# Kernel optimization log

Hardware: AMD Instinct MI355X
Metric: run time of the kernel (lower is better)

The kernel has to match this reference:

```python
import jax, jax.numpy as jnp
import numpy as np

B, C, H, W = 2, 192, 128, 128
NUM_HEADS = 6
AMP = 1
NUM_OFFSETS = 9


def bilinear_sample(img, grid):
    # img: (C, H, W); grid: (Hn, Wn, 2) in [-1,1], align_corners=True, zeros padding
    Hh, Ww = img.shape[1], img.shape[2]
    x = (grid[..., 0] + 1.0) * 0.5 * (Ww - 1)
    y = (grid[..., 1] + 1.0) * 0.5 * (Hh - 1)
    x0 = jnp.floor(x)
    y0 = jnp.floor(y)
    x1 = x0 + 1.0
    y1 = y0 + 1.0
    wx1 = x - x0
    wy1 = y - y0

    def gather(yi, xi):
        valid = ((xi >= 0) & (xi <= Ww - 1) & (yi >= 0) & (yi <= Hh - 1)).astype(img.dtype)
        xc = jnp.clip(xi, 0, Ww - 1).astype(jnp.int32)
        yc = jnp.clip(yi, 0, Hh - 1).astype(jnp.int32)
        return img[:, yc, xc] * valid  # (C, Hn, Wn)

    return (gather(y0, x0) * ((1 - wy1) * (1 - wx1))
            + gather(y0, x1) * ((1 - wy1) * wx1)
            + gather(y1, x0) * (wy1 * (1 - wx1))
            + gather(y1, x1) * (wy1 * wx1))


def setup_inputs() -> dict:
    key = jax.random.key(0)
    ks = jax.random.split(key, 8)
    s = 0.02
    Ch = C // NUM_HEADS
    return {
        "x_q": jax.random.normal(ks[0], (B, C, H, W), jnp.float32),
        "x_kv": jax.random.normal(ks[1], (B, C, H, W), jnp.float32),
        "w_q": jax.random.normal(ks[2], (C, C), jnp.float32) * s,
        "w_kv": jax.random.normal(ks[3], (2 * C, C), jnp.float32) * s,
        "w_off1": jax.random.normal(ks[4], (C, 2 * C, 3, 3), jnp.float32) * s,
        "b_off1": jnp.zeros((C,), jnp.float32),
        "w_off2": jax.random.normal(ks[5], (2 * NUM_OFFSETS, C), jnp.float32) * s,
        "b_off2": jnp.zeros((2 * NUM_OFFSETS,), jnp.float32),
        "w_proj": jax.random.normal(ks[6], (C, C), jnp.float32) * s,
        "b_proj": jnp.zeros((C,), jnp.float32),
    }


def reference(x_q, x_kv, w_q, w_kv, w_off1, b_off1, w_off2, b_off2, w_proj, b_proj):
    Ch = C // NUM_HEADS
    scale = Ch ** (-0.5)

    # 1x1 conv projections as channel matmuls
    q = jnp.einsum('oc,bchw->bohw', w_q, x_q) * scale
    kv = jnp.einsum('oc,bchw->bohw', w_kv, x_kv)
    k, v = kv[:, :C], kv[:, C:]  # kv.reshape(B,2,Ch,nh,H,W) -> first C channels are k

    # offset predictor: 3x3 conv -> relu -> 1x1 conv
    off_in = jnp.concatenate([x_q, x_kv], axis=1)
    h1 = jax.lax.conv_general_dilated(off_in, w_off1, (1, 1), 'SAME',
                                      dimension_numbers=('NCHW', 'OIHW', 'NCHW'))
    h1 = jax.nn.relu(h1 + b_off1[None, :, None, None])
    off = jnp.einsum('oc,bchw->bohw', w_off2, h1) + b_off2[None, :, None, None]
    off = off.reshape(B, NUM_OFFSETS, 2, H, W).transpose(0, 1, 3, 4, 2)  # (B,9,H,W,2)
    gx = off[..., 0] / (W - 1) * 2.0 - 1.0
    gy = off[..., 1] / (H - 1) * 2.0 - 1.0
    grid = jnp.stack([gx, gy], axis=-1)  # (B,9,H,W,2)

    # deformable gather: sample full-channel k/v at each of 9 per-pixel offset grids
    sample = jax.vmap(jax.vmap(bilinear_sample, in_axes=(None, 0)), in_axes=(0, 0))
    k_s = sample(k, grid).reshape(B, NUM_OFFSETS, Ch, NUM_HEADS, H, W)
    v_s = sample(v, grid).reshape(B, NUM_OFFSETS, Ch, NUM_HEADS, H, W)

    q = q.reshape(B, Ch, NUM_HEADS, H, W)

    pad = [(0, 0), (0, 0), (0, 0), (0, 0), (AMP, AMP), (AMP, AMP)]
    k_p = jnp.pad(k_s, pad)
    v_p = jnp.pad(v_s, pad)

    win = 2 * AMP + 1
    logits = []
    for i in range(win):
        for j in range(win):
            idx = i * win + j
            kp = k_p[:, idx, :, :, i:i + H, j:j + W]  # (B,Ch,nh,H,W)
            logits.append(jnp.einsum('bchxy,bchxy->bhxy', q, kp))
    attn = jax.nn.softmax(jnp.stack(logits, axis=1), axis=1)  # (B,9,nh,H,W)

    out = jnp.zeros((B, Ch, NUM_HEADS, H, W), x_q.dtype)
    for i in range(win):
        for j in range(win):
            idx = i * win + j
            vp = v_p[:, idx, :, :, i:i + H, j:j + W]
            out = out + attn[:, idx, None] * vp

    out = out.reshape(B, C, H, W)  # channel layout = (Ch, nh), matching torch reshape
    return jnp.einsum('oc,bchw->bohw', w_proj, out) + b_proj[None, :, None, None]
```

## Files before the change

### kernel.cpp

```cpp
#include <hip/hip_runtime.h>
#include <math.h>

#define HW 16384
#define NB 2
#define NC 192

typedef __attribute__((ext_vector_type(8))) short bh8;
typedef __attribute__((ext_vector_type(4))) float f32x4;

__device__ inline ushort f2bf(float f) {
  union { float f; unsigned int u; } x; x.f = f;
  unsigned int r = x.u + 0x7fffu + ((x.u >> 16) & 1u);
  return (ushort)(r >> 16);
}
__device__ inline float bf2f(ushort u) {
  union { unsigned int i; float f; } x; x.i = ((unsigned int)u) << 16;
  return x.f;
}
__device__ inline float asf(unsigned int u) {
  union { unsigned int i; float f; } x; x.i = u; return x.f;
}
__device__ inline unsigned int cvtpk(float lo, float hi) {
  unsigned int r;
  asm("v_cvt_pk_bf16_f32 %0, %1, %2" : "=v"(r) : "v"(lo), "v"(hi));
  return r;
}
__device__ inline void gl16(const ushort* g, char* l) {
  __builtin_amdgcn_global_load_lds(
      (const __attribute__((address_space(1))) unsigned int*)g,
      (__attribute__((address_space(3))) unsigned int*)l, 16, 0, 0);
}

__global__ void k_wpack(const float* __restrict__ w1, ushort* __restrict__ wpack) {
  int i = blockIdx.x * 256 + threadIdx.x;
  int s = i / 6144;
  int rem = i - s * 6144;
  int o = rem >> 5, kk = rem & 31;
  int dy = s / 36, t2 = s - dy * 36;
  int icc = t2 / 3, dxi = t2 - icc * 3;
  int ic = icc * 32 + kk;
  wpack[i] = f2bf(w1[(size_t)o * 3456 + (size_t)ic * 9 + dy * 3 + dxi]);
}

__global__ void k_wgpack(const float* __restrict__ wq, const float* __restrict__ wkv,
                         const float* __restrict__ wp, float scale,
                         ushort* __restrict__ wg) {
  int i = blockIdx.x * 256 + threadIdx.x;
  int r = i / NC, c = i - r * NC;
  float v;
  if (r < 192) {
    int orow = (r & 31) * 6 + (r >> 5);
    v = wq[(size_t)orow * NC + c] * scale;
  } else if (r < 576) {
    int rp = r - 192;
    int t = rp >= 192 ? 1 : 0;
    int cc = rp - t * 192;
    int orow = t * 192 + (cc & 31) * 6 + (cc >> 5);
    v = wkv[(size_t)orow * NC + c];
  } else {
    int rp = r - 576;
    v = wp[(size_t)rp * NC + ((c & 31) * 6 + (c >> 5))];
  }
  wg[i] = f2bf(v);
}

__global__ void k_zerohalo(ushort* __restrict__ xpp) {
  int i = blockIdx.x * 256 + threadIdx.x;
  int t = i / 48;
  int c = i - t * 48;
  int b = t / 520;
  int slot = t - b * 520;
  int row, px;
  if (slot < 132) { row = 0; px = slot; }
  else if (slot < 264) { row = 129; px = slot - 132; }
  else { int j = slot - 264; row = 1 + (j >> 1); px = (j & 1) ? 131 : 0; }
  *(uint4*)(xpp + ((size_t)(b * 130 + row) * 132 + px) * 384 + c * 8) =
      make_uint4(0u, 0u, 0u, 0u);
}

__global__ __launch_bounds__(256) void k_xpack(const float* __restrict__ xq,
                                               const float* __restrict__ xkv,
                                               ushort* __restrict__ xpp) {
  __shared__ float t[NC][65];
  const int tid = threadIdx.x;
  const size_t r0 = (size_t)blockIdx.x * 64;
  const int b = (int)(r0 >> 14);
  const int px0 = (int)(r0 & 16383);
  const int y = px0 >> 7, x0 = px0 & 127;
  const float* src = (blockIdx.y == 0 ? xq : xkv) + (size_t)b * NC * HW + px0;
#pragma unroll
  for (int it = 0; it < 12; ++it) {
    int i = it * 256 + tid;
    int c = i >> 4, q4 = i & 15;
    float4 v = *(const float4*)(src + (size_t)c * HW + q4 * 4);
    t[c][q4 * 4 + 0] = v.x; t[c][q4 * 4 + 1] = v.y;
    t[c][q4 * 4 + 2] = v.z; t[c][q4 * 4 + 3] = v.w;
  }
  __syncthreads();
  ushort* dst = xpp + ((size_t)(b * 130 + y + 1) * 132 + x0 + 1) * 384 +
                blockIdx.y * 192;
#pragma unroll
  for (int it = 0; it < 6; ++it) {
    int i = it * 256 + tid;
    int px = i / 24, ch = i - px * 24;
    ushort4 u0, u1;
    u0.x = f2bf(t[ch * 8 + 0][px]); u0.y = f2bf(t[ch * 8 + 1][px]);
    u0.z = f2bf(t[ch * 8 + 2][px]); u0.w = f2bf(t[ch * 8 + 3][px]);
    u1.x = f2bf(t[ch * 8 + 4][px]); u1.y = f2bf(t[ch * 8 + 5][px]);
    u1.z = f2bf(t[ch * 8 + 6][px]); u1.w = f2bf(t[ch * 8 + 7][px]);
    *(ushort4*)&dst[(size_t)px * 384 + ch * 8] = u0;
    *(ushort4*)&dst[(size_t)px * 384 + ch * 8 + 4] = u1;
  }
}

__device__ inline void stage64(ushort* lds, const ushort* src, int rowStride,
                               int tid) {
#pragma unroll
  for (int it = 0; it < 6; ++it) {
    int i = it * 256 + tid;
    int row = i / 24, c = i - row * 24;
    int pos = (c & 24) | ((c & 7) ^ (row & 7));
    uint4 v = *(const uint4*)(src + (size_t)row * rowStride + c * 8);
    *(uint4*)&lds[row * NC + pos * 8] = v;
  }
}
__device__ inline bh8 frag64(const ushort* lds, int row, int c) {
  int pos = (c & 24) | ((c & 7) ^ (row & 7));
  return *(const bh8*)&lds[row * NC + pos * 8];
}

__global__ __launch_bounds__(256) void k_gemm_mfma(
    const ushort* __restrict__ xpp, const ushort* __restrict__ wg,
    ushort* __restrict__ qb, ushort* __restrict__ kvb) {
  __shared__ __attribute__((aligned(16))) ushort xs[64 * NC];
  __shared__ __attribute__((aligned(16))) ushort ws2[64 * NC];
  const int tid = threadIdx.x;
  const size_t p0 = (size_t)blockIdx.x * 64;
  const int bb = (int)(p0 >> 14);
  const int yy = (int)((p0 >> 7) & 127);
  const int xx0 = (int)(p0 & 127);
  const int which = blockIdx.y;
  const int cOff = (which == 0) ? 0 : 192;
  const ushort* src = xpp + ((size_t)(bb * 130 + yy + 1) * 132 + xx0 + 1) * 384 + cOff;
  const ushort* wbase = wg + (size_t)(which * 192) * NC;
  stage64(xs, src, 384, tid);
  const int lid = tid & 15, g = (tid >> 4) & 3, wv = tid >> 6;
  const int wo = (wv & 1) * 32, wp = (wv >> 1) * 32;
  const int vofs = (which == 2) ? 4 : 0;
  for (int ot = 0; ot < 3; ++ot) {
    if (ot) __syncthreads();
    stage64(ws2, wbase + (size_t)(ot * 64) * NC, NC, tid);
    __syncthreads();
    f32x4 acc[2][2];
#pragma unroll
    for (int m = 0; m < 2; ++m)
#pragma unroll
      for (int n = 0; n < 2; ++n) acc[m][n] = (f32x4){0.f, 0.f, 0.f, 0.f};
#pragma unroll
    for (int k = 0; k < 6; ++k) {
      bh8 a0 = frag64(ws2, wo + lid, k * 4 + g);
      bh8 a1 = frag64(ws2, wo + 16 + lid, k * 4 + g);
      bh8 b0 = frag64(xs, wp + lid, k * 4 + g);
      bh8 b1 = frag64(xs, wp + 16 + lid, k * 4 + g);
      acc[0][0] = __builtin_amdgcn_mfma_f32_16x16x32_bf16(a0, b0, acc[0][0], 0, 0, 0);
      acc[0][1] = __builtin_amdgcn_mfma_f32_16x16x32_bf16(a0, b1, acc[0][1], 0, 0, 0);
      acc[1][0] = __builtin_amdgcn_mfma_f32_16x16x32_bf16(a1, b0, acc[1][0], 0, 0, 0);
      acc[1][1] = __builtin_amdgcn_mfma_f32_16x16x32_bf16(a1, b1, acc[1][1], 0, 0, 0);
    }
    const int od = ot * 64;
#pragma unroll
    for (int m = 0; m < 2; ++m)
#pragma unroll
      for (int n = 0; n < 2; ++n) {
        int orow = od + wo + m * 16 + g * 4;
        size_t px = p0 + wp + n * 16 + lid;
        ushort4 u;
        u.x = f2bf(acc[m][n][0]); u.y = f2bf(acc[m][n][1]);
        u.z = f2bf(acc[m][n][2]); u.w = f2bf(acc[m][n][3]);
        if (which == 0)
          *(ushort4*)&qb[px * NC + orow] = u;
        else
          *(ushort4*)&kvb[px * 384 + orow * 2 + vofs] = u;
      }
  }
}

__global__ __launch_bounds__(256) void k_proj_mfma(
    const ushort* __restrict__ pre, const ushort* __restrict__ wg,
    const float* __restrict__ bp, float* __restrict__ out) {
  __shared__ __attribute__((aligned(16))) ushort xs[64 * NC];
  __shared__ __attribute__((aligned(16))) ushort ws2[64 * NC];
  const int tid = threadIdx.x;
  const size_t p0 = (size_t)blockIdx.x * 64;
  const int o0 = blockIdx.y * 64;
  stage64(xs, pre + p0 * NC, NC, tid);
  stage64(ws2, wg + (size_t)o0 * NC, NC, tid);
  __syncthreads();
  const int lid = tid & 15, g = (tid >> 4) & 3, wv = tid >> 6;
  const int wo = (wv & 1) * 32, wp = (wv >> 1) * 32;
  f32x4 acc[2][2];
#pragma unroll
  for (int m = 0; m < 2; ++m)
#pragma unroll
    for (int n = 0; n < 2; ++n) acc[m][n] = (f32x4){0.f, 0.f, 0.f, 0.f};
#pragma unroll
  for (int k = 0; k < 6; ++k) {
    bh8 a0 = frag64(ws2, wo + lid, k * 4 + g);
    bh8 a1 = frag64(ws2, wo + 16 + lid, k * 4 + g);
    bh8 b0 = frag64(xs, wp + lid, k * 4 + g);
    bh8 b1 = frag64(xs, wp + 16 + lid, k * 4 + g);
    acc[0][0] = __builtin_amdgcn_mfma_f32_16x16x32_bf16(a0, b0, acc[0][0], 0, 0, 0);
    acc[0][1] = __builtin_amdgcn_mfma_f32_16x16x32_bf16(a0, b1, acc[0][1], 0, 0, 0);
    acc[1][0] = __builtin_amdgcn_mfma_f32_16x16x32_bf16(a1, b0, acc[1][0], 0, 0, 0);
    acc[1][1] = __builtin_amdgcn_mfma_f32_16x16x32_bf16(a1, b1, acc[1][1], 0, 0, 0);
  }
#pragma unroll
  for (int m = 0; m < 2; ++m)
#pragma unroll
    for (int n = 0; n < 2; ++n) {
      int oc = o0 + wo + m * 16 + g * 4;
      size_t pxf = p0 + wp + n * 16 + lid;
      int b = (int)(pxf >> 14);
      int px = (int)(pxf & 16383);
#pragma unroll
      for (int j = 0; j < 4; ++j)
        out[((size_t)b * NC + oc + j) * HW + px] = acc[m][n][j] + bp[oc + j];
    }
}

#define CP0 0
#define CP1 8448
#define CW0 16896
#define CW1 35328
__global__ __launch_bounds__(256, 3) void k_conv_mfma(
    const ushort* __restrict__ xpp, const ushort* __restrict__ wpack,
    const float* __restrict__ b1, ushort* __restrict__ h1) {
  __shared__ __attribute__((aligned(16))) char smem[53760];
  const int tid = threadIdx.x;
  const int bi = (blockIdx.x & 7) * 64 + (blockIdx.x >> 3);
  const int b = bi >> 8;
  const int y = (bi >> 1) & 127;
  const int oh = bi & 1;
  const int lid = tid & 15;
  const int g = (tid >> 4) & 3;
  const int wv = tid >> 6;
  const int lane = tid & 63;
  const int og = wv & 1;
  const int pg = wv >> 1;
  f32x4 acc[3][4];
#pragma unroll
  for (int m = 0; m < 3; ++m)
#pragma unroll
    for (int n = 0; n < 4; ++n) acc[m][n] = (f32x4){0.f, 0.f, 0.f, 0.f};

  auto stageP = [&](int icc, int dy, int buf) {
    const size_t rowbase = (size_t)(b * 130 + y + dy) * 132 * 384 + icc * 32;
    char* dst0 = smem + (buf ? CP1 : CP0);
    for (int grp = wv; grp < 9; grp += 4) {
      int i = grp * 64 + lane;
      if (i < 528) {
        int slot = i >> 2, ch = i & 3;
        gl16(xpp + rowbase + (size_t)slot * 384 + ((ch ^ ((slot >> 1) & 3)) << 3),
             dst0 + grp * 1024);
      }
    }
  };
  auto stageW = [&](int icc, int dy, int buf) {
    const ushort* wsrc = wpack + (size_t)((dy * 12 + icc) * 3) * 6144 + oh * 96 * 32;
    char* dst0 = smem + (buf ? CW1 : CW0);
    for (int grp = wv; grp < 18; grp += 4) {
      int i = grp * 64 + lane;
      int dxi = i / 384;
      int rem = i - dxi * 384;
      int o = rem >> 2, q = rem & 3;
      gl16(wsrc + (size_t)dxi * 6144 + o * 32 + ((q ^ ((o >> 1) & 3)) << 3),
           dst0 + grp * 1024);
    }
  };

  stageP(0, 0, 0);
  stageW(0, 0, 0);
  __syncthreads();
  int cur = 0;
  for (int s = 0; s < 36; ++s) {
    if (s < 35) {
      const int ns = s + 1;
      const int nicc = ns / 3, ndy = ns - nicc * 3;
      stageP(nicc, ndy, cur ^ 1);
      stageW(nicc, ndy, cur ^ 1);
    }
    const char* Pb = smem + (cur ? CP1 : CP0);
    const char* Wb = smem + (cur ? CW1 : CW0);
#pragma unroll
    for (int dxi = 0; dxi < 3; ++dxi) {
      bh8 af[3];
#pragma unroll
      for (int m = 0; m < 3; ++m) {
        int o = og * 48 + m * 16 + lid;
        af[m] = *(const bh8*)(Wb + ((dxi * 96 + o) << 6) +
                              ((g ^ ((o >> 1) & 3)) << 4));
      }
#pragma unroll
      for (int n = 0; n < 4; ++n) {
        int slot = pg * 64 + n * 16 + lid + dxi;
        bh8 bf = *(const bh8*)(Pb + (slot << 6) + ((g ^ ((slot >> 1) & 3)) << 4));
#pragma unroll
        for (int m = 0; m < 3; ++m)
          acc[m][n] = __builtin_amdgcn_mfma_f32_16x16x32_bf16(
              af[m], bf, acc[m][n], 0, 0, 0);
      }
    }
    __syncthreads();
    cur ^= 1;
  }

  const size_t pxbase = (size_t)(b << 14) + y * 128 + pg * 64;
#pragma unroll
  for (int m = 0; m < 3; ++m) {
    const int ob = oh * 96 + og * 48 + m * 16 + g * 4;
    float4 bv = *(const float4*)(b1 + ob);
#pragma unroll
    for (int n = 0; n < 4; ++n) {
      size_t px = pxbase + n * 16 + lid;
      h1[(size_t)(ob + 0) * (NB * HW) + px] = f2bf(fmaxf(acc[m][n][0] + bv.x, 0.f));
      h1[(size_t)(ob + 1) * (NB * HW) + px] = f2bf(fmaxf(acc[m][n][1] + bv.y, 0.f));
      h1[(size_t)(ob + 2) * (NB * HW) + px] = f2bf(fmaxf(acc[m][n][2] + bv.z, 0.f));
      h1[(size_t)(ob + 3) * (NB * HW) + px] = f2bf(fmaxf(acc[m][n][3] + bv.w, 0.f));
    }
  }
}

__global__ __launch_bounds__(256) void k_offhead(
    const ushort* __restrict__ h1, const float* __restrict__ w2,
    const float* __restrict__ b2, float* __restrict__ off) {
  __shared__ float w2l[18 * NC];
  const int tid = threadIdx.x;
  for (int i = tid; i < 18 * NC; i += 256) w2l[i] = w2[i];
  __syncthreads();
  const int px = tid & 127;
  const int jh = tid >> 7;
  const size_t p = (size_t)blockIdx.x * 128 + px;
  float acc[9];
#pragma unroll
  for (int jj = 0; jj < 9; ++jj) acc[jj] = b2[jh * 9 + jj];
  for (int c = 0; c < NC; ++c) {
    float v = bf2f(h1[(size_t)c * (NB * HW) + p]);
#pragma unroll
    for (int jj = 0; jj < 9; ++jj) acc[jj] += w2l[(jh * 9 + jj) * NC + c] * v;
  }
#pragma unroll
  for (int jj = 0; jj < 9; ++jj) off[p * 18 + jh * 9 + jj] = acc[jj];
}

__global__ __launch_bounds__(192, 6) void k_attn(
    const ushort* __restrict__ q, const ushort* __restrict__ kv,
    const float* __restrict__ off, ushort* __restrict__ pre) {
  const int s = threadIdx.x;
  const int pix = s / 48;
  const int sub = s - pix * 48;
  const int p = blockIdx.x * 4 + pix;
  const int b = p >> 14;
  const int pp = p & 16383;
  const int y = pp >> 7, x = pp & 127;

  uint2 qu = *(const uint2*)(q + (size_t)p * NC + 4 * sub);
  const float q0 = asf(qu.x << 16), q1 = asf(qu.x & 0xffff0000u);
  const float q2 = asf(qu.y << 16), q3 = asf(qu.y & 0xffff0000u);
  const ushort* kl = kv + (size_t)b * (HW * 384) + sub * 8;
  const int obase = b * HW;

  float pl[9];
  unsigned int vp0[9], vp1[9];
#pragma unroll
  for (int idx = 0; idx < 9; ++idx) {
    const int yy = y + idx / 3 - 1, xx = x + idx % 3 - 1;
    const bool inb = (yy >= 0) && (yy < 128) && (xx >= 0) && (xx < 128);
    float sx = 0.f, sy = 0.f;
    if (inb) {
      const int sp = obase + yy * 128 + xx;
      sx = off[sp * 18 + idx * 2 + 0];
      sy = off[sp * 18 + idx * 2 + 1];
    }
    const float fx0 = floorf(sx), fy0 = floorf(sy);
    const float wx1 = sx - fx0, wy1 = sy - fy0;
    const float wx0 = 1.f - wx1, wy0 = 1.f - wy1;
    const float inbf = inb ? 1.f : 0.f;
    const float wxm0 = wx0 * ((fx0 >= 0.f && fx0 <= 127.f) ? inbf : 0.f);
    const float wxm1 = wx1 * ((fx0 >= -1.f && fx0 <= 126.f) ? inbf : 0.f);
    const float wym0 = wy0 * ((fy0 >= 0.f && fy0 <= 127.f) ? 1.f : 0.f);
    const float wym1 = wy1 * ((fy0 >= -1.f && fy0 <= 126.f) ? 1.f : 0.f);
    const int ix0 = (int)fminf(fmaxf(fx0, 0.f), 127.f);
    const int iy0 = (int)fminf(fmaxf(fy0, 0.f), 127.f);
    const int ix1 = (int)fminf(fmaxf(fx0 + 1.f, 0.f), 127.f);
    const int iy1 = (int)fminf(fmaxf(fy0 + 1.f, 0.f), 127.f);
    const float w00 = wym0 * wxm0, w01 = wym0 * wxm1;
    const float w10 = wym1 * wxm0, w11 = wym1 * wxm1;
    const unsigned int e00 = (unsigned int)(iy0 * 128 + ix0) * 384u;
    const unsigned int e01 = (unsigned int)(iy0 * 128 + ix1) * 384u;
    const unsigned int e10 = (unsigned int)(iy1 * 128 + ix0) * 384u;
    const unsigned int e11 = (unsigned int)(iy1 * 128 + ix1) * 384u;
    float ks0 = 0.f, ks1 = 0.f, ks2 = 0.f, ks3 = 0.f;
    float vs0 = 0.f, vs1 = 0.f, vs2 = 0.f, vs3 = 0.f;
#define CORNER(W, E)                                            \
  {                                                             \
    uint4 kk = *(const uint4*)(kl + (E));                       \
    ks0 = fmaf((W), asf(kk.x << 16), ks0);                      \
    ks1 = fmaf((W), asf(kk.x & 0xffff0000u), ks1);              \
    ks2 = fmaf((W), asf(kk.y << 16), ks2);                      \
    ks3 = fmaf((W), asf(kk.y & 0xffff0000u), ks3);              \
    vs0 = fmaf((W), asf(kk.z << 16), vs0);                      \
    vs1 = fmaf((W), asf(kk.z & 0xffff0000u), vs1);              \
    vs2 = fmaf((W), asf(kk.w << 16), vs2);                      \
    vs3 = fmaf((W), asf(kk.w & 0xffff0000u), vs3);              \
  }
    CORNER(w00, e00)
    CORNER(w01, e01)
    CORNER(w10, e10)
    CORNER(w11, e11)
#undef CORNER
    float pd = q0 * ks0 + q1 * ks1 + q2 * ks2 + q3 * ks3;
    pd += __shfl_xor(pd, 1);
    pd += __shfl_xor(pd, 2);
    pd += __shfl_xor(pd, 4);
    pl[idx] = pd;
    vp0[idx] = cvtpk(vs0, vs1);
    vp1[idx] = cvtpk(vs2, vs3);
  }
  float mx = pl[0];
#pragma unroll
  for (int i = 1; i < 9; ++i) mx = fmaxf(mx, pl[i]);
  float sm = 0.f;
#pragma unroll
  for (int i = 0; i < 9; ++i) { pl[i] = __expf(pl[i] - mx); sm += pl[i]; }
  const float inv = __builtin_amdgcn_rcpf(sm);
  float o0 = 0.f, o1 = 0.f, o2 = 0.f, o3 = 0.f;
#pragma unroll
  for (int i = 0; i < 9; ++i) {
    const float a = pl[i] * inv;
    o0 = fmaf(a, asf(vp0[i] << 16), o0);
    o1 = fmaf(a, asf(vp0[i] & 0xffff0000u), o1);
    o2 = fmaf(a, asf(vp1[i] << 16), o2);
    o3 = fmaf(a, asf(vp1[i] & 0xffff0000u), o3);
  }
  ushort4 r;
  r.x = f2bf(o0); r.y = f2bf(o1); r.z = f2bf(o2); r.w = f2bf(o3);
  *(ushort4*)(pre + (size_t)p * NC + 4 * sub) = r;
}

extern "C" void kernel_launch(void* const* d_in, const int* in_sizes, int n_in,
                              void* d_out, int out_size, void* d_ws, size_t ws_size,
                              hipStream_t stream) {
  const float* x_q    = (const float*)d_in[0];
  const float* x_kv   = (const float*)d_in[1];
  const float* w_q    = (const float*)d_in[2];
  const float* w_kv   = (const float*)d_in[3];
  const float* w_off1 = (const float*)d_in[4];
  const float* b_off1 = (const float*)d_in[5];
  const float* w_off2 = (const float*)d_in[6];
  const float* b_off2 = (const float*)d_in[7];
  const float* w_proj = (const float*)d_in[8];
  const float* b_proj = (const float*)d_in[9];
  float* out = (float*)d_out;

  char* W = (char*)d_ws;
  const size_t SB = (size_t)NB * HW * NC * 2;
  ushort* qb   = (ushort*)W;
  ushort* kvb  = (ushort*)(W + SB);
  ushort* preb = (ushort*)(W + 3 * SB);
  ushort* h1b  = preb;
  ushort* wg   = (ushort*)(W + 4 * SB);
  float*  offb = (float*)(W + 4 * SB + 294912);
  ushort* xpp  = (ushort*)(W + 4 * SB + 294912 + 2359296);
  ushort* wpk  = (ushort*)d_out;

  const float scale = 0.17677669529663687f;
  dim3 blk(256);
  k_wpack<<<dim3(2592), blk, 0, stream>>>(w_off1, wpk);
  k_wgpack<<<dim3(576), blk, 0, stream>>>(w_q, w_kv, w_proj, scale, wg);
  k_zerohalo<<<dim3(195), blk, 0, stream>>>(xpp);
  k_xpack<<<dim3(512, 2), blk, 0, stream>>>(x_q, x_kv, xpp);
  k_gemm_mfma<<<dim3(512, 3), blk, 0, stream>>>(xpp, wg, qb, kvb);
  k_conv_mfma<<<dim3(512), blk, 0, stream>>>(xpp, wpk, b_off1, h1b);
  k_offhead<<<dim3(NB * 128), blk, 0, stream>>>(h1b, w_off2, b_off2, offb);
  k_attn<<<dim3(8192), dim3(192), 0, stream>>>(qb, kvb, offb, preb);
  k_proj_mfma<<<dim3(512, 3), blk, 0, stream>>>(preb, wg + 576 * NC, b_proj, out);
}
```

Before: 168.5 us.

## Split 3x3 offset conv reduction over input channels across two block halves

```diff
diff --git a/kernel.cpp b/kernel.cpp
--- a/kernel.cpp
+++ b/kernel.cpp
@@ -234,13 +234,17 @@
 #define CW1 35328
 __global__ __launch_bounds__(256, 3) void k_conv_mfma(
     const ushort* __restrict__ xpp, const ushort* __restrict__ wpack,
-    const float* __restrict__ b1, ushort* __restrict__ h1) {
+    const float* __restrict__ b1, ushort* __restrict__ h1a,
+    ushort* __restrict__ h1b) {
   __shared__ __attribute__((aligned(16))) char smem[53760];
   const int tid = threadIdx.x;
-  const int bi = (blockIdx.x & 7) * 64 + (blockIdx.x >> 3);
+  const int logical = (blockIdx.x & 7) * 128 + (blockIdx.x >> 3);
+  const int half = logical >> 9;
+  const int bi = logical & 511;
   const int b = bi >> 8;
   const int y = (bi >> 1) & 127;
   const int oh = bi & 1;
+  const int iccB = half * 6;
   const int lid = tid & 15;
   const int g = (tid >> 4) & 3;
   const int wv = tid >> 6;
@@ -278,14 +282,14 @@
     }
   };
 
-  stageP(0, 0, 0);
-  stageW(0, 0, 0);
+  stageP(iccB, 0, 0);
+  stageW(iccB, 0, 0);
   __syncthreads();
   int cur = 0;
-  for (int s = 0; s < 36; ++s) {
-    if (s < 35) {
+  for (int s = 0; s < 18; ++s) {
+    if (s < 17) {
       const int ns = s + 1;
-      const int nicc = ns / 3, ndy = ns - nicc * 3;
+      const int nicc = iccB + ns / 3, ndy = ns - (ns / 3) * 3;
       stageP(nicc, ndy, cur ^ 1);
       stageW(nicc, ndy, cur ^ 1);
     }
@@ -314,25 +318,27 @@
     cur ^= 1;
   }
 
+  ushort* dst = half ? h1b : h1a;
   const size_t pxbase = (size_t)(b << 14) + y * 128 + pg * 64;
 #pragma unroll
   for (int m = 0; m < 3; ++m) {
     const int ob = oh * 96 + og * 48 + m * 16 + g * 4;
-    float4 bv = *(const float4*)(b1 + ob);
+    float4 bv = half ? make_float4(0.f, 0.f, 0.f, 0.f) : *(const float4*)(b1 + ob);
 #pragma unroll
     for (int n = 0; n < 4; ++n) {
       size_t px = pxbase + n * 16 + lid;
-      h1[(size_t)(ob + 0) * (NB * HW) + px] = f2bf(fmaxf(acc[m][n][0] + bv.x, 0.f));
-      h1[(size_t)(ob + 1) * (NB * HW) + px] = f2bf(fmaxf(acc[m][n][1] + bv.y, 0.f));
-      h1[(size_t)(ob + 2) * (NB * HW) + px] = f2bf(fmaxf(acc[m][n][2] + bv.z, 0.f));
-      h1[(size_t)(ob + 3) * (NB * HW) + px] = f2bf(fmaxf(acc[m][n][3] + bv.w, 0.f));
+      dst[(size_t)(ob + 0) * (NB * HW) + px] = f2bf(acc[m][n][0] + bv.x);
+      dst[(size_t)(ob + 1) * (NB * HW) + px] = f2bf(acc[m][n][1] + bv.y);
+      dst[(size_t)(ob + 2) * (NB * HW) + px] = f2bf(acc[m][n][2] + bv.z);
+      dst[(size_t)(ob + 3) * (NB * HW) + px] = f2bf(acc[m][n][3] + bv.w);
     }
   }
 }
 
 __global__ __launch_bounds__(256) void k_offhead(
-    const ushort* __restrict__ h1, const float* __restrict__ w2,
-    const float* __restrict__ b2, float* __restrict__ off) {
+    const ushort* __restrict__ h1a, const ushort* __restrict__ h1b,
+    const float* __restrict__ w2, const float* __restrict__ b2,
+    float* __restrict__ off) {
   __shared__ float w2l[18 * NC];
   const int tid = threadIdx.x;
   for (int i = tid; i < 18 * NC; i += 256) w2l[i] = w2[i];
@@ -344,7 +350,8 @@
 #pragma unroll
   for (int jj = 0; jj < 9; ++jj) acc[jj] = b2[jh * 9 + jj];
   for (int c = 0; c < NC; ++c) {
-    float v = bf2f(h1[(size_t)c * (NB * HW) + p]);
+    float v = fmaxf(bf2f(h1a[(size_t)c * (NB * HW) + p]) +
+                    bf2f(h1b[(size_t)c * (NB * HW) + p]), 0.f);
 #pragma unroll
     for (int jj = 0; jj < 9; ++jj) acc[jj] += w2l[(jh * 9 + jj) * NC + c] * v;
   }
@@ -467,10 +474,11 @@
   ushort* qb   = (ushort*)W;
   ushort* kvb  = (ushort*)(W + SB);
   ushort* preb = (ushort*)(W + 3 * SB);
-  ushort* h1b  = preb;
+  ushort* h1a  = preb;
   ushort* wg   = (ushort*)(W + 4 * SB);
   float*  offb = (float*)(W + 4 * SB + 294912);
   ushort* xpp  = (ushort*)(W + 4 * SB + 294912 + 2359296);
+  ushort* h1b  = (ushort*)(W + 4 * SB + 294912 + 2359296 + 26357760);
   ushort* wpk  = (ushort*)d_out;
 
   const float scale = 0.17677669529663687f;
@@ -480,8 +488,8 @@
   k_zerohalo<<<dim3(195), blk, 0, stream>>>(xpp);
   k_xpack<<<dim3(512, 2), blk, 0, stream>>>(x_q, x_kv, xpp);
   k_gemm_mfma<<<dim3(512, 3), blk, 0, stream>>>(xpp, wg, qb, kvb);
-  k_conv_mfma<<<dim3(512), blk, 0, stream>>>(xpp, wpk, b_off1, h1b);
-  k_offhead<<<dim3(NB * 128), blk, 0, stream>>>(h1b, w_off2, b_off2, offb);
+  k_conv_mfma<<<dim3(1024), blk, 0, stream>>>(xpp, wpk, b_off1, h1a, h1b);
+  k_offhead<<<dim3(NB * 128), blk, 0, stream>>>(h1a, h1b, w_off2, b_off2, offb);
   k_attn<<<dim3(8192), dim3(192), 0, stream>>>(qb, kvb, offb, preb);
   k_proj_mfma<<<dim3(512, 3), blk, 0, stream>>>(preb, wg + 576 * NC, b_proj, out);
 }
```

After: 234.8 us. +39.3%, slower.
